# Kernel tuning notes

Measured on AMD Instinct MI355X. Metric: run time of the kernel, lower is better.

The kernel has to match this reference:

```python
import jax, jax.numpy as jnp
import numpy as np

ALPHA = 0.25
GAMMA = 2.0
EPS = 1e-8


def _lsa(cost):
    """Jonker-Volgenant shortest-augmenting-path linear sum assignment.
    Matches scipy.optimize.linear_sum_assignment for rectangular matrices."""
    cost = np.asarray(cost, dtype=np.float64)
    transposed = cost.shape[0] > cost.shape[1]
    if transposed:
        cost = cost.T
    n, m = cost.shape  # n <= m
    INF = 1e18
    u = np.zeros(n + 1)
    v = np.zeros(m + 1)
    p = np.zeros(m + 1, dtype=np.int64)   # p[j] = row (1-indexed) assigned to col j
    way = np.zeros(m + 1, dtype=np.int64)
    for i in range(1, n + 1):
        p[0] = i
        j0 = 0
        minv = np.full(m + 1, INF)
        used = np.zeros(m + 1, dtype=bool)
        while True:
            used[j0] = True
            i0 = p[j0]
            cur = cost[i0 - 1] - u[i0] - v[1:]
            free = ~used[1:]
            better = free & (cur < minv[1:])
            minv[1:][better] = cur[better]
            way[1:][better] = j0
            masked = np.where(free, minv[1:], INF)
            j1 = int(np.argmin(masked)) + 1
            delta = masked[j1 - 1]
            u[p[used]] += delta
            v[used] -= delta
            minv[1:][free] -= delta
            j0 = j1
            if p[j0] == 0:
                break
        while j0 != 0:  # augment
            j1 = way[j0]
            p[j0] = p[j1]
            j0 = j1
    row_of_col = p[1:] - 1
    cols = np.nonzero(row_of_col >= 0)[0]
    rows = row_of_col[cols]
    if transposed:
        rows, cols = cols, rows
    order = np.argsort(rows)
    return rows[order], cols[order]


def _focal_cost(p):
    """pos_cost - neg_cost for sigmoid probs p, per focal-loss matcher cost."""
    neg = (1.0 - ALPHA) * p ** GAMMA * (-jnp.log(1.0 - p + EPS))
    pos = ALPHA * (1.0 - p) ** GAMMA * (-jnp.log(p + EPS))
    return pos - neg


def _match(rec, loc, targets):
    """rec: [bs, Q, Crec] logits; loc: [bs, Q, Cloc] logits; targets: [bs, nt] int.
    Returns (src_idx, tgt_idx) each [bs, nt] (query index, target index)."""
    nt = targets.shape[1]
    cost_class = jnp.take_along_axis(_focal_cost(jax.nn.sigmoid(rec)),
                                     targets[:, None, :], axis=2)      # [bs, Q, nt]
    cost_pos = _focal_cost(jax.nn.sigmoid(loc))[:, :, :nt]             # tgt_pos = arange(nt)
    C = np.asarray(2.0 * cost_class + cost_pos)                        # [bs, Q, nt]
    src, tgt = [], []
    for b in range(C.shape[0]):  # per-batch Hungarian, as in original
        r, c = _lsa(C[b])
        src.append(r)
        tgt.append(c)
    return jnp.asarray(np.stack(src)), jnp.asarray(np.stack(tgt))


def _ce(logits, labels):
    # F.cross_entropy with mean reduction
    logp = jax.nn.log_softmax(logits, axis=-1)
    return -jnp.mean(jnp.take_along_axis(logp, labels[..., None], axis=-1))


def setup_inputs() -> dict:
    key = jax.random.key(0)
    k1, k2, k3 = jax.random.split(key, 3)
    rec = jax.random.normal(k1, (128, 107, 32, 32), dtype=jnp.float32)
    loc = jax.random.normal(k2, (128, 25, 32, 32), dtype=jnp.float32)
    targets = jax.random.randint(k3, (128, 25), 0, 107, dtype=jnp.int64)
    return {"rec": rec, "loc": loc, "targets": targets}


def reference(rec, loc, targets):
    bs, c_rec, H, W = rec.shape
    c_loc = loc.shape[1]
    nt = targets.shape[1]
    rec = jnp.transpose(rec.reshape(bs, c_rec, H * W), (0, 2, 1))  # [bs, Q, Crec]
    loc = jnp.transpose(loc.reshape(bs, c_loc, H * W), (0, 2, 1))  # [bs, Q, Cloc]
    src_idx, tgt_idx = _match(rec, loc, targets)                   # [bs, nt] each
    rec_m = jnp.take_along_axis(rec, src_idx[:, :, None], axis=1)  # [bs, nt, Crec]
    loc_m = jnp.take_along_axis(loc, src_idx[:, :, None], axis=1)  # [bs, nt, Cloc]
    cls_labels = jnp.take_along_axis(targets, tgt_idx, axis=1)     # [bs, nt]
    pos_labels = tgt_idx                                           # tgt_pos[b, j] == j
    det_rec_losses = _ce(rec_m.reshape(bs * nt, c_rec), cls_labels.reshape(-1))
    pos_losses = _ce(loc_m.reshape(bs * nt, c_loc), pos_labels.reshape(-1))
    return (det_rec_losses, pos_losses)
```

## Files before the change

### kernel.cpp

```cpp
#include <hip/hip_runtime.h>
#include <hip/hip_bf16.h>
#include <math.h>

#define BS   128
#define NT   25
#define CREC 107
#define CLOC 25
#define QN   1024
#define INFD 1e18
#define WSTR 257
__device__ __forceinline__ int widx(int j) {
    int q = j - 1;
    return (q & 3) * WSTR + (q >> 2);
}

__device__ __forceinline__ float focal_cost_f(float x) {
    float p   = 1.0f / (1.0f + __expf(-x));
    float neg = 0.75f * p * p * (-__logf(1.0f - p + 1e-8f));
    float pos = 0.25f * (1.0f - p) * (1.0f - p) * (-__logf(p + 1e-8f));
    return pos - neg;
}

__global__ __launch_bounds__(256)
void search_kernel(const float* __restrict__ rec, const float* __restrict__ loc,
                   const int* __restrict__ targets, int* __restrict__ pairq_g) {
    extern __shared__ float cost_s[];
    const int b     = blockIdx.x;
    const int tid   = threadIdx.x;
    const int wave  = tid >> 6;
    const int lane  = tid & 63;
    const int qbase = tid << 2;

    __shared__ int    way_s[3 * WSTR + 256];
    __shared__ int    p_s[QN + 1];
    __shared__ double u_s[NT + 1];
    __shared__ int    t_s[NT];
    __shared__ float  bmv_s[NT][4];
    __shared__ int    bmq_s[NT][4];
    __shared__ float  rowmin_s[NT];
    __shared__ int    rowarg_s[NT];
    __shared__ int    unassigned_s[NT];
    __shared__ int    nun_s;
    __shared__ double candv_s[2][4];
    __shared__ int    candj_s[2][4];

    for (int j = tid; j <= QN; j += 256) p_s[j] = 0;
    if (tid < NT) t_s[tid] = targets[b * NT + tid];
    __syncthreads();

    const size_t rb0 = (size_t)b * CREC * QN;
    const size_t lb0 = (size_t)b * CLOC * QN;

    {
        float4 ra = *(const float4*)(rec + rb0 + (size_t)t_s[0] * QN + qbase);
        float4 la = *(const float4*)(loc + lb0 + qbase);
        for (int r = 0; r < NT; ++r) {
            float4 rn, ln;
            if (r + 1 < NT) {
                rn = *(const float4*)(rec + rb0 + (size_t)t_s[r + 1] * QN + qbase);
                ln = *(const float4*)(loc + lb0 + (size_t)(r + 1) * QN + qbase);
            }
            float4 c;
            c.x = 2.0f * focal_cost_f(ra.x) + focal_cost_f(la.x);
            c.y = 2.0f * focal_cost_f(ra.y) + focal_cost_f(la.y);
            c.z = 2.0f * focal_cost_f(ra.z) + focal_cost_f(la.z);
            c.w = 2.0f * focal_cost_f(ra.w) + focal_cost_f(la.w);
            *(float4*)(cost_s + (r << 10) + qbase) = c;
            if (r + 1 < NT) { ra = rn; la = ln; }
        }
    }
    __syncthreads();

    for (int r = 0; r < NT; ++r) {
        float4 c = *(const float4*)(cost_s + (r << 10) + qbase);
        float bv = c.x; int bq = qbase;
        if (c.y < bv) { bv = c.y; bq = qbase + 1; }
        if (c.z < bv) { bv = c.z; bq = qbase + 2; }
        if (c.w < bv) { bv = c.w; bq = qbase + 3; }
        #pragma unroll
        for (int off = 32; off; off >>= 1) {
            float ov = __shfl_xor(bv, off);
            int   oq = __shfl_xor(bq, off);
            if (ov < bv || (ov == bv && oq < bq)) { bv = ov; bq = oq; }
        }
        if (lane == 0) { bmv_s[r][wave] = bv; bmq_s[r][wave] = bq; }
    }
    __syncthreads();
    if (tid < NT) {
        float bv = bmv_s[tid][0]; int bq = bmq_s[tid][0];
        #pragma unroll
        for (int w = 1; w < 4; ++w) {
            float ov = bmv_s[tid][w]; int oq = bmq_s[tid][w];
            if (ov < bv || (ov == bv && oq < bq)) { bv = ov; bq = oq; }
        }
        rowmin_s[tid] = bv; rowarg_s[tid] = bq;
    }
    __syncthreads();
    if (tid == 0) {
        nun_s = 0;
        for (int r = 0; r < NT; ++r) {
            u_s[r + 1] = (double)rowmin_s[r];
            int j = rowarg_s[r] + 1;
            if (p_s[j] == 0) p_s[j] = r + 1;
            else             unassigned_s[nun_s++] = r + 1;
        }
    }
    __syncthreads();
    const int nun = nun_s;

    double v[4] = {0.0, 0.0, 0.0, 0.0};

    for (int s = 0; s < nun; ++s) {
        const int i = unassigned_s[s];
        double minv[4] = {INFD, INFD, INFD, INFD};
        double snap[4] = {0.0, 0.0, 0.0, 0.0};
        double dsum    = 0.0;
        unsigned usedmask = 0;
        int j0 = 0;
        int parity = 0;

        for (;;) {
            int i0;
            if (j0 == 0) {
                i0 = i;
            } else {
                int q0 = j0 - 1;
                if ((q0 >> 2) == tid) {
                    int m = q0 & 3;
                    usedmask |= 1u << m;
                    minv[m] = INFD;
                    snap[m] = dsum;
                }
                i0 = p_s[j0];
            }
            const double ui0 = u_s[i0];
            const float4 c4 = *(const float4*)(cost_s + ((i0 - 1) << 10) + qbase);
            const float cf[4] = { c4.x, c4.y, c4.z, c4.w };

            double bestv = INFD; int bestj = QN + 2;
            #pragma unroll
            for (int m = 0; m < 4; ++m) {
                if (!(usedmask & (1u << m))) {
                    const int j = qbase + m + 1;
                    double cur = (double)cf[m] - ui0 - v[m];
                    if (cur < minv[m]) { minv[m] = cur; way_s[widx(j)] = j0; }
                    double mv = minv[m];
                    if (mv < bestv || (mv == bestv && j < bestj)) { bestv = mv; bestj = j; }
                }
            }
            #pragma unroll
            for (int off = 32; off; off >>= 1) {
                double ov = __shfl_xor(bestv, off);
                int    oj = __shfl_xor(bestj, off);
                if (ov < bestv || (ov == bestv && oj < bestj)) { bestv = ov; bestj = oj; }
            }
            if (lane == 0) { candv_s[parity][wave] = bestv; candj_s[parity][wave] = bestj; }
            __syncthreads();
            double delta = candv_s[parity][0]; int j1 = candj_s[parity][0];
            #pragma unroll
            for (int w = 1; w < 4; ++w) {
                double dv = candv_s[parity][w]; int dj = candj_s[parity][w];
                if (dv < delta || (dv == delta && dj < j1)) { delta = dv; j1 = dj; }
            }
            parity ^= 1;
            dsum += delta;

            #pragma unroll
            for (int m = 0; m < 4; ++m) {
                if (usedmask & (1u << m)) v[m]    -= delta;
                else                      minv[m] -= delta;
            }
            j0 = j1;
            if (p_s[j0] == 0) break;
        }

        if (tid == 0) u_s[i] += dsum;
        unsigned mm = usedmask;
        while (mm) {
            int m = __ffs(mm) - 1; mm &= mm - 1;
            u_s[p_s[qbase + m + 1]] += dsum - snap[m];
        }
        __syncthreads();
        if (tid == 0) {
            int jj = j0;
            while (jj != 0) {
                int jn = way_s[widx(jj)];
                p_s[jj] = (jn == 0) ? i : p_s[jn];
                jj = jn;
            }
        }
        __syncthreads();
    }

    for (int j = tid + 1; j <= QN; j += 256)
        if (p_s[j] > 0) pairq_g[b * NT + (p_s[j] - 1)] = j - 1;
}

__global__ __launch_bounds__(64)
void loss_kernel(const float* __restrict__ rec, const float* __restrict__ loc,
                 const int* __restrict__ targets, const int* __restrict__ pairq_g,
                 float* __restrict__ partial) {
    const int pid  = blockIdx.x;
    const int b    = pid / NT, t = pid % NT;
    const int lane = threadIdx.x;
    const int q    = pairq_g[pid];

    const float* rb = rec + (size_t)b * CREC * QN + q;
    float x0 = (lane < CREC)      ? rb[(size_t)lane * QN]        : -1e30f;
    float x1 = (lane + 64 < CREC) ? rb[(size_t)(lane + 64) * QN] : -1e30f;
    float mx = fmaxf(x0, x1);
    #pragma unroll
    for (int off = 32; off; off >>= 1) mx = fmaxf(mx, __shfl_xor(mx, off));
    float e = 0.0f;
    if (lane < CREC)      e += expf(x0 - mx);
    if (lane + 64 < CREC) e += expf(x1 - mx);
    #pragma unroll
    for (int off = 32; off; off >>= 1) e += __shfl_xor(e, off);
    float lse = mx + logf(e);

    const float* lb = loc + (size_t)b * CLOC * QN + q;
    float y = (lane < CLOC) ? lb[(size_t)lane * QN] : -1e30f;
    float my = y;
    #pragma unroll
    for (int off = 32; off; off >>= 1) my = fmaxf(my, __shfl_xor(my, off));
    float ey = (lane < CLOC) ? expf(y - my) : 0.0f;
    #pragma unroll
    for (int off = 32; off; off >>= 1) ey += __shfl_xor(ey, off);
    float lsey = my + logf(ey);

    if (lane == 0) {
        int lab = targets[pid];
        partial[pid]           = lse  - rb[(size_t)lab * QN];
        partial[BS * NT + pid] = lsey - lb[(size_t)t * QN];
    }
}

__global__ __launch_bounds__(256)
void finalize_kernel(const float* __restrict__ partial, float* __restrict__ out) {
    const int tid = threadIdx.x;
    float s0 = 0.0f, s1 = 0.0f;
    for (int i = tid; i < BS * NT; i += 256) {
        s0 += partial[i];
        s1 += partial[BS * NT + i];
    }
    __shared__ float a0[4], a1[4];
    #pragma unroll
    for (int off = 32; off; off >>= 1) { s0 += __shfl_xor(s0, off); s1 += __shfl_xor(s1, off); }
    if ((tid & 63) == 0) { a0[tid >> 6] = s0; a1[tid >> 6] = s1; }
    __syncthreads();
    if (tid == 0) {
        out[0] = (a0[0] + a0[1] + a0[2] + a0[3]) * (1.0f / (BS * NT));
        out[1] = (a1[0] + a1[1] + a1[2] + a1[3]) * (1.0f / (BS * NT));
    }
}

extern "C" void kernel_launch(void* const* d_in, const int* in_sizes, int n_in,
                              void* d_out, int out_size, void* d_ws, size_t ws_size,
                              hipStream_t stream) {
    (void)in_sizes; (void)n_in; (void)out_size; (void)ws_size;
    const float* rec     = (const float*)d_in[0];
    const float* loc     = (const float*)d_in[1];
    const int*   targets = (const int*)d_in[2];
    float* out = (float*)d_out;

    int*   pairq_g = (int*)d_ws;
    float* partial = (float*)(pairq_g + BS * NT);

    const int tile_bytes = NT * QN * (int)sizeof(float);
    (void)hipFuncSetAttribute((const void*)search_kernel,
                              hipFuncAttributeMaxDynamicSharedMemorySize, tile_bytes);

    hipLaunchKernelGGL(search_kernel, dim3(BS), dim3(256), tile_bytes, stream,
                       rec, loc, targets, pairq_g);
    hipLaunchKernelGGL(loss_kernel, dim3(BS * NT), dim3(64), 0, stream,
                       rec, loc, targets, pairq_g, partial);
    hipLaunchKernelGGL(finalize_kernel, dim3(1), dim3(256), 0, stream,
                       partial, out);
}
```

Before: 167.5 us.

## Run augmenting-path search in a single wavefront to drop block barriers

The Hungarian augmenting-path loop now runs on one 64-lane wavefront, with each lane holding 16 columns. This removes the per-iteration __syncthreads and the shared-memory exchange of candidates across four waves. The argmin uses a float shuffle-min plus a ballot over the tied lanes to pick the exact double minimum. Snap values move to shared memory, and the row-min pass batches five rows per shuffle reduction. The cost is that only a quarter of the threads are active during the search, and register pressure rises from the 16-wide double arrays.

New measurement: 158.5 us. -5.4%, faster.

```diff
diff --git a/kernel.cpp b/kernel.cpp
--- a/kernel.cpp
+++ b/kernel.cpp
@@ -21,7 +21,7 @@
     return pos - neg;
 }
 
-__global__ __launch_bounds__(256)
+__global__ __launch_bounds__(256, 1)
 void search_kernel(const float* __restrict__ rec, const float* __restrict__ loc,
                    const int* __restrict__ targets, int* __restrict__ pairq_g) {
     extern __shared__ float cost_s[];
@@ -31,9 +31,10 @@
     const int lane  = tid & 63;
     const int qbase = tid << 2;
 
-    __shared__ int    way_s[3 * WSTR + 256];
+    __shared__ int    way_s[4 * WSTR];
     __shared__ int    p_s[QN + 1];
     __shared__ double u_s[NT + 1];
+    __shared__ double snap_s[QN];
     __shared__ int    t_s[NT];
     __shared__ float  bmv_s[NT][4];
     __shared__ int    bmq_s[NT][4];
@@ -41,8 +42,6 @@
     __shared__ int    rowarg_s[NT];
     __shared__ int    unassigned_s[NT];
     __shared__ int    nun_s;
-    __shared__ double candv_s[2][4];
-    __shared__ int    candj_s[2][4];
 
     for (int j = tid; j <= QN; j += 256) p_s[j] = 0;
     if (tid < NT) t_s[tid] = targets[b * NT + tid];
@@ -71,19 +70,30 @@
     }
     __syncthreads();
 
-    for (int r = 0; r < NT; ++r) {
-        float4 c = *(const float4*)(cost_s + (r << 10) + qbase);
-        float bv = c.x; int bq = qbase;
-        if (c.y < bv) { bv = c.y; bq = qbase + 1; }
-        if (c.z < bv) { bv = c.z; bq = qbase + 2; }
-        if (c.w < bv) { bv = c.w; bq = qbase + 3; }
+    for (int r0 = 0; r0 < NT; r0 += 5) {
+        float bv[5]; int bq[5];
+        #pragma unroll
+        for (int rr = 0; rr < 5; ++rr) {
+            float4 c = *(const float4*)(cost_s + ((r0 + rr) << 10) + qbase);
+            float v = c.x; int q = qbase;
+            if (c.y < v) { v = c.y; q = qbase + 1; }
+            if (c.z < v) { v = c.z; q = qbase + 2; }
+            if (c.w < v) { v = c.w; q = qbase + 3; }
+            bv[rr] = v; bq[rr] = q;
+        }
         #pragma unroll
         for (int off = 32; off; off >>= 1) {
-            float ov = __shfl_xor(bv, off);
-            int   oq = __shfl_xor(bq, off);
-            if (ov < bv || (ov == bv && oq < bq)) { bv = ov; bq = oq; }
-        }
-        if (lane == 0) { bmv_s[r][wave] = bv; bmq_s[r][wave] = bq; }
+            #pragma unroll
+            for (int rr = 0; rr < 5; ++rr) {
+                float ov = __shfl_xor(bv[rr], off);
+                int   oq = __shfl_xor(bq[rr], off);
+                if (ov < bv[rr] || (ov == bv[rr] && oq < bq[rr])) { bv[rr] = ov; bq[rr] = oq; }
+            }
+        }
+        if (lane == 0) {
+            #pragma unroll
+            for (int rr = 0; rr < 5; ++rr) { bmv_s[r0 + rr][wave] = bv[rr]; bmq_s[r0 + rr][wave] = bq[rr]; }
+        }
     }
     __syncthreads();
     if (tid < NT) {
@@ -108,89 +118,102 @@
     __syncthreads();
     const int nun = nun_s;
 
-    double v[4] = {0.0, 0.0, 0.0, 0.0};
-
-    for (int s = 0; s < nun; ++s) {
-        const int i = unassigned_s[s];
-        double minv[4] = {INFD, INFD, INFD, INFD};
-        double snap[4] = {0.0, 0.0, 0.0, 0.0};
-        double dsum    = 0.0;
-        unsigned usedmask = 0;
-        int j0 = 0;
-        int parity = 0;
-
-        for (;;) {
-            int i0;
-            if (j0 == 0) {
-                i0 = i;
-            } else {
-                int q0 = j0 - 1;
-                if ((q0 >> 2) == tid) {
-                    int m = q0 & 3;
-                    usedmask |= 1u << m;
-                    minv[m] = INFD;
-                    snap[m] = dsum;
-                }
-                i0 = p_s[j0];
-            }
-            const double ui0 = u_s[i0];
-            const float4 c4 = *(const float4*)(cost_s + ((i0 - 1) << 10) + qbase);
-            const float cf[4] = { c4.x, c4.y, c4.z, c4.w };
-
-            double bestv = INFD; int bestj = QN + 2;
+    if (wave == 0 && nun > 0) {
+        double v[16], minv[16];
+        #pragma unroll
+        for (int k = 0; k < 16; ++k) v[k] = 0.0;
+
+        for (int s = 0; s < nun; ++s) {
+            const int i = unassigned_s[s];
             #pragma unroll
-            for (int m = 0; m < 4; ++m) {
-                if (!(usedmask & (1u << m))) {
-                    const int j = qbase + m + 1;
-                    double cur = (double)cf[m] - ui0 - v[m];
-                    if (cur < minv[m]) { minv[m] = cur; way_s[widx(j)] = j0; }
-                    double mv = minv[m];
-                    if (mv < bestv || (mv == bestv && j < bestj)) { bestv = mv; bestj = j; }
-                }
-            }
-            #pragma unroll
-            for (int off = 32; off; off >>= 1) {
-                double ov = __shfl_xor(bestv, off);
-                int    oj = __shfl_xor(bestj, off);
-                if (ov < bestv || (ov == bestv && oj < bestj)) { bestv = ov; bestj = oj; }
-            }
-            if (lane == 0) { candv_s[parity][wave] = bestv; candj_s[parity][wave] = bestj; }
-            __syncthreads();
-            double delta = candv_s[parity][0]; int j1 = candj_s[parity][0];
-            #pragma unroll
-            for (int w = 1; w < 4; ++w) {
-                double dv = candv_s[parity][w]; int dj = candj_s[parity][w];
-                if (dv < delta || (dv == delta && dj < j1)) { delta = dv; j1 = dj; }
-            }
-            parity ^= 1;
-            dsum += delta;
-
-            #pragma unroll
-            for (int m = 0; m < 4; ++m) {
-                if (usedmask & (1u << m)) v[m]    -= delta;
-                else                      minv[m] -= delta;
-            }
-            j0 = j1;
-            if (p_s[j0] == 0) break;
-        }
-
-        if (tid == 0) u_s[i] += dsum;
-        unsigned mm = usedmask;
-        while (mm) {
-            int m = __ffs(mm) - 1; mm &= mm - 1;
-            u_s[p_s[qbase + m + 1]] += dsum - snap[m];
-        }
-        __syncthreads();
-        if (tid == 0) {
-            int jj = j0;
-            while (jj != 0) {
-                int jn = way_s[widx(jj)];
-                p_s[jj] = (jn == 0) ? i : p_s[jn];
-                jj = jn;
-            }
-        }
-        __syncthreads();
-    }
+            for (int k = 0; k < 16; ++k) minv[k] = INFD;
+            unsigned usedmask = 0;
+            double dsum = 0.0;
+            int j0 = 0;
+
+            for (;;) {
+                int i0;
+                if (j0 == 0) {
+                    i0 = i;
+                } else {
+                    int q0 = j0 - 1;
+                    if (((q0 & 255) >> 2) == lane) {
+                        int kk = ((q0 >> 8) << 2) | (q0 & 3);
+                        #pragma unroll
+                        for (int k = 0; k < 16; ++k)
+                            if (k == kk) { usedmask |= 1u << k; minv[k] = INFD; }
+                        snap_s[q0] = dsum;
+                    }
+                    i0 = p_s[j0];
+                }
+                const double ui0 = u_s[i0];
+                const float* crow = cost_s + ((i0 - 1) << 10);
+                float cf[16];
+                #pragma unroll
+                for (int g = 0; g < 4; ++g) {
+                    float4 c4 = *(const float4*)(crow + 4 * lane + 256 * g);
+                    cf[4 * g + 0] = c4.x; cf[4 * g + 1] = c4.y;
+                    cf[4 * g + 2] = c4.z; cf[4 * g + 3] = c4.w;
+                }
+
+                double bestv = INFD; int bestj = QN + 2;
+                #pragma unroll
+                for (int k = 0; k < 16; ++k) {
+                    if (!(usedmask & (1u << k))) {
+                        const int j = 1 + 4 * lane + (k & 3) + 256 * (k >> 2);
+                        double cur = (double)cf[k] - ui0 - v[k];
+                        if (cur < minv[k]) { minv[k] = cur; way_s[widx(j)] = j0; }
+                        double mv = minv[k];
+                        if (mv < bestv || (mv == bestv && j < bestj)) { bestv = mv; bestj = j; }
+                    }
+                }
+
+                float own = (float)bestv;
+                float red = own;
+                #pragma unroll
+                for (int off = 32; off; off >>= 1) red = fminf(red, __shfl_xor(red, off));
+                unsigned long long mask = __ballot(own == red);
+                double gv = INFD; int gj = QN + 2;
+                while (mask) {
+                    int l = __ffsll(mask) - 1; mask &= mask - 1;
+                    double vv = __shfl(bestv, l);
+                    int    jj = __shfl(bestj, l);
+                    if (vv < gv || (vv == gv && jj < gj)) { gv = vv; gj = jj; }
+                }
+                const double delta = gv;
+                const int j1 = gj;
+                dsum += delta;
+
+                #pragma unroll
+                for (int k = 0; k < 16; ++k) {
+                    if (usedmask & (1u << k)) v[k]    -= delta;
+                    else                      minv[k] -= delta;
+                }
+                j0 = j1;
+                if (p_s[j0] == 0) break;
+            }
+            __threadfence_block();
+
+            if (lane == 0) u_s[i] += dsum;
+            unsigned mm = usedmask;
+            while (mm) {
+                int k = __ffs(mm) - 1; mm &= mm - 1;
+                int q = 4 * lane + (k & 3) + 256 * (k >> 2);
+                u_s[p_s[q + 1]] += dsum - snap_s[q];
+            }
+            __threadfence_block();
+            if (lane == 0) {
+                int jj = j0;
+                while (jj != 0) {
+                    int jn = way_s[widx(jj)];
+                    p_s[jj] = (jn == 0) ? i : p_s[jn];
+                    jj = jn;
+                }
+            }
+            __threadfence_block();
+        }
+    }
+    __syncthreads();
 
     for (int j = tid + 1; j <= QN; j += 256)
         if (p_s[j] > 0) pairq_g[b * NT + (p_s[j] - 1)] = j - 1;
```
